# Optimization experiments

Hardware: AMD Instinct MI355X
Metric: run time of the kernel (lower is better)

The kernel has to match this reference:

```python
import jax, jax.numpy as jnp
import numpy as np

T, B, E, H, V, L = 64, 64, 512, 1024, 10000, 2


def setup_inputs() -> dict:
    key = jax.random.key(0)
    ks = jax.random.split(key, 24)
    k = 1.0 / np.sqrt(H)
    u = lambda kk, shape, s: jax.random.uniform(kk, shape, jnp.float32, -s, s)
    return {
        "inputs": jax.random.randint(ks[0], (T, B), 0, V, dtype=jnp.int32),
        "hidden": jnp.zeros((L, B, H), jnp.float32),
        "emb": u(ks[1], (V, E), 0.1),
        "Wr0": u(ks[2], (H, E), k),
        "Wz0": u(ks[3], (H, E), k),
        "Wh0": u(ks[4], (H, E), k),
        "WrR": u(ks[5], (L - 1, H, H), k),
        "WzR": u(ks[6], (L - 1, H, H), k),
        "WhR": u(ks[7], (L - 1, H, H), k),
        "brR": u(ks[8], (L - 1, H), k),
        "bzR": u(ks[9], (L - 1, H), k),
        "bhR": u(ks[10], (L - 1, H), k),
        "Ur": u(ks[11], (L, H, H), k),
        "Uz": u(ks[12], (L, H, H), k),
        "Uh": u(ks[13], (L, H, H), k),
        "bur": u(ks[14], (L, H), k),
        "buz": u(ks[15], (L, H), k),
        "buh": u(ks[16], (L, H), k),
        "Wout": u(ks[17], (V, H), 0.1),
        "bout": jnp.zeros((V,), jnp.float32),
    }


def reference(inputs, hidden, emb, Wr0, Wz0, Wh0, WrR, WzR, WhR, brR, bzR, bhR,
              Ur, Uz, Uh, bur, buz, buh, Wout, bout):
    num_layers = hidden.shape[0]
    x_emb = emb[inputs]  # [T, B, E]

    def step(h_prev, x_t):  # h_prev [L,B,H], x_t [B,E]
        x = x_t
        hs = []
        for l in range(num_layers):
            if l == 0:
                rx = x @ Wr0.T  # layer-0 W* have no bias
                zx = x @ Wz0.T
                hx = x @ Wh0.T
            else:
                rx = x @ WrR[l - 1].T + brR[l - 1]
                zx = x @ WzR[l - 1].T + bzR[l - 1]
                hx = x @ WhR[l - 1].T + bhR[l - 1]
            hl = h_prev[l]
            r = jax.nn.sigmoid(rx + hl @ Ur[l].T + bur[l])
            z = jax.nn.sigmoid(zx + hl @ Uz[l].T + buz[l])
            h_tilda = jnp.tanh(hx + (r * hl) @ Uh[l].T + buh[l])
            h_new = (1.0 - z) * hl + z * h_tilda
            hs.append(h_new)
            x = h_new
        logits_t = x @ Wout.T + bout  # [B, V]
        return jnp.stack(hs), logits_t

    h_final, logits = jax.lax.scan(step, hidden, x_emb)
    return logits, h_final  # logits [T,B,V], h_final [L,B,H]
```

## Files before the change

kernel.cpp:

```cpp
#include <hip/hip_runtime.h>
#include <hip/hip_bf16.h>

#define T_ 64
#define B_ 64
#define E_ 512
#define H_ 1024
#define V_ 10000
#define TB 4096
#define BH 65536

typedef unsigned short u16;
typedef unsigned int u32;
typedef unsigned long long u64;
typedef __attribute__((ext_vector_type(8))) short short8v;
typedef __attribute__((ext_vector_type(4))) float f32x4;

__device__ inline f32x4 mfma_bf16(short8v a, short8v b, f32x4 c) {
  return __builtin_amdgcn_mfma_f32_16x16x32_bf16(a, b, c, 0, 0, 0);
}

__device__ inline u16 f2bf(float f) {
  unsigned u = __float_as_uint(f);
  unsigned r = (u + 0x7fffu + ((u >> 16) & 1u)) >> 16;
  return (u16)r;
}
__device__ inline float bf2f(u16 h) { return __uint_as_float(((unsigned)h) << 16); }


__global__ void k_prepall(const float* __restrict__ Wr0, const float* __restrict__ Wz0,
                          const float* __restrict__ Wh0, const float* __restrict__ Ur,
                          const float* __restrict__ Uz, const float* __restrict__ Uh,
                          const float* __restrict__ WrR, const float* __restrict__ WzR,
                          const float* __restrict__ WhR, const float* __restrict__ Wout,
                          u16* __restrict__ W0cat, u16* __restrict__ U0cat,
                          u16* __restrict__ U1W, u16* __restrict__ Woutb) {
  const int HE = H_ * E_;
  const int HH = H_ * H_;
  const size_t n0 = 3u * (size_t)HE;
  const size_t n1 = n0 + 3u * (size_t)HH;
  const size_t n2 = n1 + 3072u * 2048u;
  const size_t n3 = n2 + (size_t)V_ * H_;
  size_t i = (size_t)blockIdx.x * 256 + threadIdx.x;
  const size_t stride = (size_t)gridDim.x * 256;
  for (; i < n3; i += stride) {
    if (i < n0) {
      int g = (int)(i >> 19), off = (int)(i & (HE - 1));
      const float* s = g == 0 ? Wr0 : (g == 1 ? Wz0 : Wh0);
      W0cat[i] = f2bf(s[off]);
    } else if (i < n1) {
      size_t j = i - n0;
      int g = (int)(j >> 20), off = (int)(j & (HH - 1));
      const float* s = g == 0 ? Ur : (g == 1 ? Uz : Uh);
      U0cat[j] = f2bf(s[off]);
    } else if (i < n2) {
      size_t k = i - n1;
      int row = (int)(k >> 11), kk = (int)(k & 2047);
      int g = row >> 10, jj = row & 1023;
      const float* su = g == 0 ? Ur : (g == 1 ? Uz : Uh);
      const float* sw = g == 0 ? WrR : (g == 1 ? WzR : WhR);
      float v = (kk < 1024) ? su[(size_t)HH + (size_t)jj * 1024 + kk]
                            : sw[(size_t)jj * 1024 + (kk - 1024)];
      U1W[k] = f2bf(v);
    } else {
      size_t m = i - n2;
      Woutb[m] = f2bf(Wout[m]);
    }
  }
}

__global__ void k_gather(const int* __restrict__ idx, const float* __restrict__ emb,
                         u16* __restrict__ xbf) {
  int i = blockIdx.x * 256 + threadIdx.x;
  int row = i >> 9, e = i & 511;
  xbf[i] = f2bf(emb[(size_t)idx[row] * E_ + e]);
}

__global__ void k_bias(const float* __restrict__ bur, const float* __restrict__ buz,
                       const float* __restrict__ buh, const float* __restrict__ brR,
                       const float* __restrict__ bzR, const float* __restrict__ bhR,
                       float* __restrict__ bias0, float* __restrict__ bias1) {
  int j = blockIdx.x * 256 + threadIdx.x;
  int seg = j >> 10, col = j & 1023;
  float b0, b1;
  if (seg == 0)      { b0 = bur[col]; b1 = brR[col] + bur[H_ + col]; }
  else if (seg == 1) { b0 = buz[col]; b1 = bzR[col] + buz[H_ + col]; }
  else               { b0 = buh[col]; b1 = bhR[col] + buh[H_ + col]; }
  bias0[j] = b0; bias1[j] = b1;
}

__global__ void k_init(const float* __restrict__ hidden, u16* __restrict__ h0P,
                       u16* __restrict__ h1P) {
  int i = blockIdx.x * 256 + threadIdx.x;
  int row = i >> 10, j = i & 1023;
  int dst = ((j >> 4) << 10) + (row << 4) + (j & 15);
  h0P[dst] = f2bf(hidden[i]);
  h1P[dst] = f2bf(hidden[BH + i]);
}


__global__ __launch_bounds__(256, 2) void k_gemmX(const u16* __restrict__ A,
                                                  const u16* __restrict__ Wt,
                                                  const float* __restrict__ bias,
                                                  u16* __restrict__ XP) {
  const int m0 = blockIdx.x * 128, n0 = blockIdx.y * 128;
  const int wid = threadIdx.x >> 6, lane = threadIdx.x & 63;
  const int wm = wid >> 1, wn = wid & 1;
  const int lrow = lane & 15, lk = (lane >> 4) * 8;
  f32x4 acc[4][4] = {};
  const u16* Ab = A + (size_t)(m0 + wm * 64 + lrow) * 512 + lk;
  const u16* Wb = Wt + (size_t)(n0 + wn * 64 + lrow) * 512 + lk;
  for (int ks = 0; ks < 512; ks += 32) {
    short8v a[4], b[4];
#pragma unroll
    for (int f = 0; f < 4; f++) a[f] = *(const short8v*)(Ab + (size_t)f * 16 * 512 + ks);
#pragma unroll
    for (int f = 0; f < 4; f++) b[f] = *(const short8v*)(Wb + (size_t)f * 16 * 512 + ks);
#pragma unroll
    for (int i = 0; i < 4; i++)
#pragma unroll
      for (int j = 0; j < 4; j++) acc[i][j] = mfma_bf16(a[i], b[j], acc[i][j]);
  }
  const int drow0 = (lane >> 4) * 4, dcol = lane & 15;
#pragma unroll
  for (int i = 0; i < 4; i++)
#pragma unroll
    for (int j = 0; j < 4; j++) {
      int col = n0 + wn * 64 + j * 16 + dcol;
      float bv = bias[col];
      int g = col >> 10, cg = (col & 1023) >> 4, cc = col & 15;
#pragma unroll
      for (int v = 0; v < 4; v++) {
        int row = m0 + wm * 64 + i * 16 + drow0 + v;
        int t = row >> 6, rr = row & 63;
        XP[(((size_t)t * 64 + cg) * 64 + rr) * 48 + g * 16 + cc] = f2bf(acc[i][j][v] + bv);
      }
    }
}


__global__ __launch_bounds__(256, 2) void k_gemmL(const u16* __restrict__ AP,
                                                  const u16* __restrict__ Wt,
                                                  const float* __restrict__ bias,
                                                  float* __restrict__ C) {
  const int xcd = blockIdx.x & 7, idx = blockIdx.x >> 3;
  const int nt = xcd * 10 + (idx % 10);
  const int mt = idx / 10;
  if (nt >= 79) return;
  const int m0 = mt * 128, n0 = nt * 128;
  const int wid = threadIdx.x >> 6, lane = threadIdx.x & 63;
  const int wm = wid >> 1, wn = wid & 1;
  const int lrow = lane & 15, lk = (lane >> 4) * 8;
  const int lkb = lk >> 4, lkc = lk & 15;
  f32x4 acc[4][4] = {};
  const int rowhi = (m0 + wm * 64) >> 6;
  const u16* Ab = AP + (size_t)rowhi * BH + (size_t)lkb * 1024 + lrow * 16 + lkc;
  const u16* Wb = Wt + (size_t)(n0 + wn * 64 + lrow) * 1024 + lk;
  bool nvalid[4];
#pragma unroll
  for (int f = 0; f < 4; f++) nvalid[f] = (n0 + wn * 64 + f * 16 + lrow) < V_;
  const short8v zv = {};
  for (int ks = 0; ks < 1024; ks += 32) {
    short8v a[4], b[4];
#pragma unroll
    for (int f = 0; f < 4; f++) a[f] = *(const short8v*)(Ab + ks * 64 + f * 256);
#pragma unroll
    for (int f = 0; f < 4; f++)
      b[f] = nvalid[f] ? *(const short8v*)(Wb + (size_t)f * 16 * 1024 + ks) : zv;
#pragma unroll
    for (int i = 0; i < 4; i++)
#pragma unroll
      for (int j = 0; j < 4; j++) acc[i][j] = mfma_bf16(a[i], b[j], acc[i][j]);
  }
  const int drow0 = (lane >> 4) * 4, dcol = lane & 15;
#pragma unroll
  for (int i = 0; i < 4; i++)
#pragma unroll
    for (int j = 0; j < 4; j++) {
      int col = n0 + wn * 64 + j * 16 + dcol;
      if (col >= V_) continue;
      float bv = bias[col];
#pragma unroll
      for (int v = 0; v < 4; v++) {
        int row = m0 + wm * 64 + i * 16 + drow0 + v;
        C[(size_t)row * V_ + col] = acc[i][j][v] + bv;
      }
    }
}


__device__ inline void waitge(int* c, int tgt) {
  while (__hip_atomic_load(c, __ATOMIC_RELAXED, __HIP_MEMORY_SCOPE_AGENT) < tgt)
    __builtin_amdgcn_s_sleep(1);
}

__global__ __launch_bounds__(256, 1) void k_recur(
    const u16* __restrict__ U0, const u16* __restrict__ U1W,
    const u16* __restrict__ XP, const float* __restrict__ bias1,
    const float* __restrict__ hidden,
    u16* __restrict__ h0P, u16* __restrict__ h1P,
    u16* __restrict__ r0P, u16* __restrict__ r1P,
    int* __restrict__ flags, float* __restrict__ hfin) {
  __shared__ __align__(16) u16 wlds[65536];

  const int tid = threadIdx.x, gbid = blockIdx.x;
  int* bcast0 = flags + 4096;
  int* bcast1 = flags + 4128;

  if (gbid >= 128) {
    const int layA = gbid - 128;
    int* slots = flags + layA * 2048;
    int* bc = layA ? bcast1 : bcast0;
    if (tid < 64) {
      int* myslot = slots + tid * 32;
      int last = 0;
      for (int ph = 1; ph <= 2 * T_; ph++) {
        while (last < ph) {
          last = __hip_atomic_load(myslot, __ATOMIC_RELAXED, __HIP_MEMORY_SCOPE_AGENT);
          if (last < ph) __builtin_amdgcn_s_sleep(1);
        }
        if (tid == 0)
          __hip_atomic_store(bc, ph, __ATOMIC_RELAXED, __HIP_MEMORY_SCOPE_AGENT);
      }
    }
    return;
  }

  const int lay = gbid >> 6;
  const int cg = gbid & 63;
  const int jr = cg * 16;
  const int wid = tid >> 6, lane = tid & 63;
  const int lrow = lane & 15, lk = (lane >> 4) * 8;
  const int lk3 = lk >> 3, x7 = lrow & 7;
  const int drow0 = (lane >> 4) * 4, dcol = lane & 15;
  const int abase = (lk >> 4) * 1024 + (wid * 16 + lrow) * 16 + (lk & 15);
  const int KLS = lay ? 11 : 10;
  int* myslot = flags + lay * 2048 + cg * 32;

  {
    const u16* Wg = lay ? U1W : U0;
    const int lCPR = lay ? 8 : 7;
    const int NG = lay ? 2 : 3;
    const int total = NG << (4 + lCPR);
    const int KL = 1 << KLS;
    for (int idx = tid; idx < total; idx += 256) {
      int r16 = idx >> lCPR;
      int ch = idx & ((1 << lCPR) - 1);
      int g = r16 >> 4, r = r16 & 15;
      short8v v = *(const short8v*)(Wg + (size_t)((g << 10) + jr + r) * KL + (ch << 3));
      *(short8v*)&wlds[((size_t)r16 << KLS) + ((ch ^ (r & 7)) << 3)] = v;
    }
  }
  __syncthreads();

  const int lbR = lrow << KLS;
  const int lbZ = (16 + lrow) << KLS;
  const int lbH = (32 + lrow) << KLS;
  const u16* Whg = U1W + (size_t)(2048 + jr + lrow) * 2048 + lk;
  const int orow = wid * 16 + drow0;

  float hreg[4];
#pragma unroll
  for (int v = 0; v < 4; v++)
    hreg[v] = hidden[(size_t)lay * BH + (size_t)(orow + v) * 1024 + jr + dcol];

  if (!lay) {
    for (int t = 0; t < T_; t++) {
      float xr[4], xz[4], xh[4], zreg[4];
      const u16* xb = XP + (((size_t)t * 64 + cg) * 64 + orow) * 48 + dcol;
#pragma unroll
      for (int v = 0; v < 4; v++) {
        xr[v] = bf2f(xb[v * 48]);
        xz[v] = bf2f(xb[v * 48 + 16]);
        xh[v] = bf2f(xb[v * 48 + 32]);
      }
      if (t) { if (tid == 0) waitge(bcast0, 2 * t); __syncthreads(); }
      f32x4 ar = {}, az = {};
      {
        const u16* Ab = h0P + (size_t)t * BH + abase;
        short8v av[32];
#pragma unroll
        for (int i = 0; i < 32; i++) av[i] = *(const short8v*)(Ab + i * 2048);
#pragma unroll
        for (int i = 0; i < 32; i++) {
          const int sw = (((i * 4) + lk3) ^ x7) << 3;
          ar = mfma_bf16(av[i], *(short8v*)&wlds[lbR + sw], ar);
          az = mfma_bf16(av[i], *(short8v*)&wlds[lbZ + sw], az);
        }
      }
      u16* rtile = r0P + (size_t)t * BH + (size_t)cg * 1024;
#pragma unroll
      for (int v = 0; v < 4; v++) {
        float r = 1.f / (1.f + __expf(-(ar[v] + xr[v])));
        float z = 1.f / (1.f + __expf(-(az[v] + xz[v])));
        zreg[v] = z;
        u16 me = f2bf(r * hreg[v]);
        int oth = __shfl_xor((int)me, 1);
        if (!(dcol & 1)) {
          u32 pk = (u32)me | ((u32)(u16)oth << 16);
          __hip_atomic_store((u32*)(rtile + (orow + v) * 16 + dcol), pk,
                             __ATOMIC_RELAXED, __HIP_MEMORY_SCOPE_AGENT);
        }
      }
      asm volatile("s_waitcnt vmcnt(0)" ::: "memory");
      __syncthreads();
      if (tid == 0) {
        __hip_atomic_store(myslot, 2 * t + 1, __ATOMIC_RELAXED, __HIP_MEMORY_SCOPE_AGENT);
        waitge(bcast0, 2 * t + 1);
      }
      __syncthreads();
      f32x4 ah = {};
      {
        const u16* Abr = r0P + (size_t)t * BH + abase;
        short8v av[32];
#pragma unroll
        for (int i = 0; i < 32; i++) av[i] = *(const short8v*)(Abr + i * 2048);
#pragma unroll
        for (int i = 0; i < 32; i++) {
          const int sw = (((i * 4) + lk3) ^ x7) << 3;
          ah = mfma_bf16(av[i], *(short8v*)&wlds[lbH + sw], ah);
        }
      }
      u16* htile = h0P + (size_t)(t + 1) * BH + (size_t)cg * 1024;
#pragma unroll
      for (int v = 0; v < 4; v++) {
        float th = tanhf(ah[v] + xh[v]);
        float hn = (1.f - zreg[v]) * hreg[v] + zreg[v] * th;
        hreg[v] = hn;
        u16 me = f2bf(hn);
        int oth = __shfl_xor((int)me, 1);
        if (!(dcol & 1)) {
          u32 pk = (u32)me | ((u32)(u16)oth << 16);
          __hip_atomic_store((u32*)(htile + (orow + v) * 16 + dcol), pk,
                             __ATOMIC_RELAXED, __HIP_MEMORY_SCOPE_AGENT);
        }
        if (t == T_ - 1)
          hfin[(size_t)(orow + v) * 1024 + jr + dcol] = hn;
      }
      asm volatile("s_waitcnt vmcnt(0)" ::: "memory");
      __syncthreads();
      if (tid == 0)
        __hip_atomic_store(myslot, 2 * t + 2, __ATOMIC_RELAXED, __HIP_MEMORY_SCOPE_AGENT);
    }
  } else {
    float bR = bias1[jr + dcol];
    float bZ = bias1[1024 + jr + dcol];
    float bH = bias1[2048 + jr + dcol];
    if (tid == 0) waitge(bcast0, 2);
    __syncthreads();
    for (int t = 0; t < T_; t++) {
      float zreg[4];
      const u16* Ab0 = h0P + (size_t)(t + 1) * BH + abase;
      f32x4 ar = {}, az = {};
      {
        short8v av[32];
#pragma unroll
        for (int i = 0; i < 32; i++) av[i] = *(const short8v*)(Ab0 + i * 2048);
#pragma unroll
        for (int i = 0; i < 32; i++) {
          const int sw = ((128 + i * 4 + lk3) ^ x7) << 3;
          ar = mfma_bf16(av[i], *(short8v*)&wlds[lbR + sw], ar);
          az = mfma_bf16(av[i], *(short8v*)&wlds[lbZ + sw], az);
        }
      }
      if (tid == 0) {
        if (t) waitge(bcast1, 2 * t);
        int tgt = 2 * (t + 2);
        waitge(bcast0, tgt > 2 * T_ ? 2 * T_ : tgt);
      }
      __syncthreads();
      {
        const u16* Ab1 = h1P + (size_t)t * BH + abase;
        short8v av[32];
#pragma unroll
        for (int i = 0; i < 32; i++) av[i] = *(const short8v*)(Ab1 + i * 2048);
#pragma unroll
        for (int i = 0; i < 32; i++) {
          const int sw = ((i * 4 + lk3) ^ x7) << 3;
          ar = mfma_bf16(av[i], *(short8v*)&wlds[lbR + sw], ar);
          az = mfma_bf16(av[i], *(short8v*)&wlds[lbZ + sw], az);
        }
      }
      u16* rtile = r1P + (size_t)t * BH + (size_t)cg * 1024;
#pragma unroll
      for (int v = 0; v < 4; v++) {
        float r = 1.f / (1.f + __expf(-(ar[v] + bR)));
        float z = 1.f / (1.f + __expf(-(az[v] + bZ)));
        zreg[v] = z;
        u16 me = f2bf(r * hreg[v]);
        int oth = __shfl_xor((int)me, 1);
        if (!(dcol & 1)) {
          u32 pk = (u32)me | ((u32)(u16)oth << 16);
          __hip_atomic_store((u32*)(rtile + (orow + v) * 16 + dcol), pk,
                             __ATOMIC_RELAXED, __HIP_MEMORY_SCOPE_AGENT);
        }
      }
      asm volatile("s_waitcnt vmcnt(0)" ::: "memory");
      __syncthreads();
      if (tid == 0)
        __hip_atomic_store(myslot, 2 * t + 1, __ATOMIC_RELAXED, __HIP_MEMORY_SCOPE_AGENT);
      f32x4 ah = {};
      {
        short8v av[32];
#pragma unroll
        for (int i = 0; i < 32; i++) av[i] = *(const short8v*)(Ab0 + i * 2048);
#pragma unroll
        for (int i = 0; i < 32; i++)
          ah = mfma_bf16(av[i], *(const short8v*)(Whg + 1024 + i * 32), ah);
      }
      if (tid == 0) waitge(bcast1, 2 * t + 1);
      __syncthreads();
      {
        const u16* Abr = r1P + (size_t)t * BH + abase;
        short8v av[32];
#pragma unroll
        for (int i = 0; i < 32; i++) av[i] = *(const short8v*)(Abr + i * 2048);
#pragma unroll
        for (int i = 0; i < 32; i++)
          ah = mfma_bf16(av[i], *(const short8v*)(Whg + i * 32), ah);
      }
      u16* htile = h1P + (size_t)(t + 1) * BH + (size_t)cg * 1024;
#pragma unroll
      for (int v = 0; v < 4; v++) {
        float th = tanhf(ah[v] + bH);
        float hn = (1.f - zreg[v]) * hreg[v] + zreg[v] * th;
        hreg[v] = hn;
        u16 me = f2bf(hn);
        int oth = __shfl_xor((int)me, 1);
        if (!(dcol & 1)) {
          u32 pk = (u32)me | ((u32)(u16)oth << 16);
          __hip_atomic_store((u32*)(htile + (orow + v) * 16 + dcol), pk,
                             __ATOMIC_RELAXED, __HIP_MEMORY_SCOPE_AGENT);
        }
        if (t == T_ - 1)
          hfin[(size_t)BH + (size_t)(orow + v) * 1024 + jr + dcol] = hn;
      }
      asm volatile("s_waitcnt vmcnt(0)" ::: "memory");
      __syncthreads();
      if (tid == 0)
        __hip_atomic_store(myslot, 2 * t + 2, __ATOMIC_RELAXED, __HIP_MEMORY_SCOPE_AGENT);
    }
  }
}


extern "C" void kernel_launch(void* const* d_in, const int* in_sizes, int n_in,
                              void* d_out, int out_size, void* d_ws, size_t ws_size,
                              hipStream_t stream) {
  const int* inputs = (const int*)d_in[0];
  const float* hidden = (const float*)d_in[1];
  const float* emb = (const float*)d_in[2];
  const float* Wr0 = (const float*)d_in[3];
  const float* Wz0 = (const float*)d_in[4];
  const float* Wh0 = (const float*)d_in[5];
  const float* WrR = (const float*)d_in[6];
  const float* WzR = (const float*)d_in[7];
  const float* WhR = (const float*)d_in[8];
  const float* brR = (const float*)d_in[9];
  const float* bzR = (const float*)d_in[10];
  const float* bhR = (const float*)d_in[11];
  const float* Ur = (const float*)d_in[12];
  const float* Uz = (const float*)d_in[13];
  const float* Uh = (const float*)d_in[14];
  const float* bur = (const float*)d_in[15];
  const float* buz = (const float*)d_in[16];
  const float* buh = (const float*)d_in[17];
  const float* Wout = (const float*)d_in[18];
  const float* bout = (const float*)d_in[19];
  float* out = (float*)d_out;

  char* ws = (char*)d_ws;
  size_t off = 0;
  auto alloc = [&](size_t bytes) -> void* {
    void* p = ws + off;
    off += (bytes + 255) & ~(size_t)255;
    return p;
  };
  u16* x_bf  = (u16*)alloc((size_t)TB * E_ * 2);
  u16* W0cat = (u16*)alloc((size_t)3072 * 512 * 2);
  u16* U0cat = (u16*)alloc((size_t)3072 * 1024 * 2);
  u16* U1W   = (u16*)alloc((size_t)3072 * 2048 * 2);
  u16* Woutb = (u16*)alloc((size_t)V_ * H_ * 2);
  float* bias0 = (float*)alloc(3072 * 4);
  float* bias1 = (float*)alloc(3072 * 4);
  u16* XP    = (u16*)alloc((size_t)TB * 3072 * 2);
  u16* h0P   = (u16*)alloc((size_t)(T_ + 1) * BH * 2);
  u16* h1P   = (u16*)alloc((size_t)(T_ + 1) * BH * 2);
  u16* r0P   = (u16*)alloc((size_t)T_ * BH * 2);
  u16* r1P   = (u16*)alloc((size_t)T_ * BH * 2);
  int* flags = (int*)alloc(32768);
  (void)ws_size; (void)in_sizes; (void)n_in; (void)out_size;

  hipMemsetAsync(flags, 0, 32768, stream);

  k_prepall<<<2048, 256, 0, stream>>>(Wr0, Wz0, Wh0, Ur, Uz, Uh, WrR, WzR, WhR, Wout,
                                      W0cat, U0cat, U1W, Woutb);
  k_gather<<<TB * E_ / 256, 256, 0, stream>>>(inputs, emb, x_bf);
  k_bias<<<12, 256, 0, stream>>>(bur, buz, buh, brR, bzR, bhR, bias0, bias1);
  k_init<<<256, 256, 0, stream>>>(hidden, h0P, h1P);

  k_gemmX<<<dim3(32, 24), 256, 0, stream>>>(x_bf, W0cat, bias0, XP);
  k_recur<<<130, 256, 0, stream>>>(U0cat, U1W, XP, bias1, hidden, h0P, h1P,
                                   r0P, r1P, flags, out + (size_t)TB * V_);
  k_gemmL<<<2560, 256, 0, stream>>>(h1P + BH, Woutb, bout, out);
}
```

Measured before the change: 1.469 ms.

## Replace aggregator broadcast blocks with wave-wide direct polling of per-block flags

Removes the two aggregator blocks that gathered per-block phase flags and republished them as a broadcast counter. Each worker block now has its first wave poll all 64 peer slots at once and use a wave vote to decide when to proceed. This removes one extra hop of cross-CU latency per barrier phase. It also keeps the layer-0 hidden operand of layer 1 in registers so it is reused for the candidate-gate MFMA instead of being reloaded. The cost is more polling traffic, since 128 blocks each poll 64 flags, and higher register pressure from holding 32 vectors across a barrier.

```diff
diff --git a/kernel.cpp b/kernel.cpp
--- a/kernel.cpp
+++ b/kernel.cpp
@@ -188,9 +188,14 @@
 }
 
 
-__device__ inline void waitge(int* c, int tgt) {
-  while (__hip_atomic_load(c, __ATOMIC_RELAXED, __HIP_MEMORY_SCOPE_AGENT) < tgt)
-    __builtin_amdgcn_s_sleep(1);
+__device__ inline void pollall(const int* slots, int tgt) {
+  const int lane = threadIdx.x & 63;
+  const int* p = slots + lane * 32;
+  for (;;) {
+    int v = __hip_atomic_load(p, __ATOMIC_RELAXED, __HIP_MEMORY_SCOPE_AGENT);
+    if (__all(v >= tgt)) break;
+    __builtin_amdgcn_s_sleep(2);
+  }
 }
 
 __global__ __launch_bounds__(256, 1) void k_recur(
@@ -203,28 +208,6 @@
   __shared__ __align__(16) u16 wlds[65536];
 
   const int tid = threadIdx.x, gbid = blockIdx.x;
-  int* bcast0 = flags + 4096;
-  int* bcast1 = flags + 4128;
-
-  if (gbid >= 128) {
-    const int layA = gbid - 128;
-    int* slots = flags + layA * 2048;
-    int* bc = layA ? bcast1 : bcast0;
-    if (tid < 64) {
-      int* myslot = slots + tid * 32;
-      int last = 0;
-      for (int ph = 1; ph <= 2 * T_; ph++) {
-        while (last < ph) {
-          last = __hip_atomic_load(myslot, __ATOMIC_RELAXED, __HIP_MEMORY_SCOPE_AGENT);
-          if (last < ph) __builtin_amdgcn_s_sleep(1);
-        }
-        if (tid == 0)
-          __hip_atomic_store(bc, ph, __ATOMIC_RELAXED, __HIP_MEMORY_SCOPE_AGENT);
-      }
-    }
-    return;
-  }
-
   const int lay = gbid >> 6;
   const int cg = gbid & 63;
   const int jr = cg * 16;
@@ -234,7 +217,9 @@
   const int drow0 = (lane >> 4) * 4, dcol = lane & 15;
   const int abase = (lk >> 4) * 1024 + (wid * 16 + lrow) * 16 + (lk & 15);
   const int KLS = lay ? 11 : 10;
-  int* myslot = flags + lay * 2048 + cg * 32;
+  int* f0s = flags;
+  int* f1s = flags + 2048;
+  int* myslot = (lay ? f1s : f0s) + cg * 32;
 
   {
     const u16* Wg = lay ? U1W : U0;
@@ -273,7 +258,7 @@
         xz[v] = bf2f(xb[v * 48 + 16]);
         xh[v] = bf2f(xb[v * 48 + 32]);
       }
-      if (t) { if (tid == 0) waitge(bcast0, 2 * t); __syncthreads(); }
+      if (t) { if (tid < 64) pollall(f0s, 2 * t); __syncthreads(); }
       f32x4 ar = {}, az = {};
       {
         const u16* Ab = h0P + (size_t)t * BH + abase;
@@ -303,10 +288,9 @@
       }
       asm volatile("s_waitcnt vmcnt(0)" ::: "memory");
       __syncthreads();
-      if (tid == 0) {
+      if (tid == 0)
         __hip_atomic_store(myslot, 2 * t + 1, __ATOMIC_RELAXED, __HIP_MEMORY_SCOPE_AGENT);
-        waitge(bcast0, 2 * t + 1);
-      }
+      if (tid < 64) pollall(f0s, 2 * t + 1);
       __syncthreads();
       f32x4 ah = {};
       {
@@ -345,27 +329,25 @@
     float bR = bias1[jr + dcol];
     float bZ = bias1[1024 + jr + dcol];
     float bH = bias1[2048 + jr + dcol];
-    if (tid == 0) waitge(bcast0, 2);
+    if (tid < 64) pollall(f0s, 2);
     __syncthreads();
     for (int t = 0; t < T_; t++) {
       float zreg[4];
       const u16* Ab0 = h0P + (size_t)(t + 1) * BH + abase;
       f32x4 ar = {}, az = {};
-      {
-        short8v av[32];
-#pragma unroll
-        for (int i = 0; i < 32; i++) av[i] = *(const short8v*)(Ab0 + i * 2048);
-#pragma unroll
-        for (int i = 0; i < 32; i++) {
-          const int sw = ((128 + i * 4 + lk3) ^ x7) << 3;
-          ar = mfma_bf16(av[i], *(short8v*)&wlds[lbR + sw], ar);
-          az = mfma_bf16(av[i], *(short8v*)&wlds[lbZ + sw], az);
-        }
-      }
-      if (tid == 0) {
-        if (t) waitge(bcast1, 2 * t);
+      short8v av0[32];
+#pragma unroll
+      for (int i = 0; i < 32; i++) av0[i] = *(const short8v*)(Ab0 + i * 2048);
+#pragma unroll
+      for (int i = 0; i < 32; i++) {
+        const int sw = ((128 + i * 4 + lk3) ^ x7) << 3;
+        ar = mfma_bf16(av0[i], *(short8v*)&wlds[lbR + sw], ar);
+        az = mfma_bf16(av0[i], *(short8v*)&wlds[lbZ + sw], az);
+      }
+      if (tid < 64) {
+        if (t) pollall(f1s, 2 * t);
         int tgt = 2 * (t + 2);
-        waitge(bcast0, tgt > 2 * T_ ? 2 * T_ : tgt);
+        pollall(f0s, tgt > 2 * T_ ? 2 * T_ : tgt);
       }
       __syncthreads();
       {
@@ -399,15 +381,10 @@
       if (tid == 0)
         __hip_atomic_store(myslot, 2 * t + 1, __ATOMIC_RELAXED, __HIP_MEMORY_SCOPE_AGENT);
       f32x4 ah = {};
-      {
-        short8v av[32];
-#pragma unroll
-        for (int i = 0; i < 32; i++) av[i] = *(const short8v*)(Ab0 + i * 2048);
-#pragma unroll
-        for (int i = 0; i < 32; i++)
-          ah = mfma_bf16(av[i], *(const short8v*)(Whg + 1024 + i * 32), ah);
-      }
-      if (tid == 0) waitge(bcast1, 2 * t + 1);
+#pragma unroll
+      for (int i = 0; i < 32; i++)
+        ah = mfma_bf16(av0[i], *(const short8v*)(Whg + 1024 + i * 32), ah);
+      if (tid < 64) pollall(f1s, 2 * t + 1);
       __syncthreads();
       {
         const u16* Abr = r1P + (size_t)t * BH + abase;
@@ -499,7 +476,7 @@
   k_init<<<256, 256, 0, stream>>>(hidden, h0P, h1P);
 
   k_gemmX<<<dim3(32, 24), 256, 0, stream>>>(x_bf, W0cat, bias0, XP);
-  k_recur<<<130, 256, 0, stream>>>(U0cat, U1W, XP, bias1, hidden, h0P, h1P,
+  k_recur<<<128, 256, 0, stream>>>(U0cat, U1W, XP, bias1, hidden, h0P, h1P,
                                    r0P, r1P, flags, out + (size_t)TB * V_);
   k_gemmL<<<2560, 256, 0, stream>>>(h1P + BH, Woutb, bout, out);
 }
```

New measurement: 1.389 ms. -5.4%, faster.
